# Performance work log

Measured on AMD Instinct MI355X. Metric: run time of the kernel, lower is better.

The kernel has to match this reference:

```python
import math
import jax, jax.numpy as jnp
import numpy as np

B, L = 2, 4096
D_MODEL, D_STATE, D_CONV, EXPAND = 1024, 64, 4, 2
D_INNER = EXPAND * D_MODEL
DT_RANK = max(1, D_MODEL // 16)
EPS = float(jnp.finfo(jnp.float32).eps)  # torch nn.RMSNorm default eps


def setup_inputs() -> dict:
    key = jax.random.key(0)
    ks = jax.random.split(key, 8)
    sc = lambda k, shape, scale: jax.random.normal(k, shape, jnp.float32) * scale
    x = jax.random.normal(ks[0], (B, L, D_MODEL), jnp.float32)
    in_proj_w = sc(ks[1], (2 * D_INNER, D_MODEL), D_MODEL ** -0.5)
    conv_w = sc(ks[2], (D_INNER, 1, D_CONV), D_CONV ** -0.5)  # depthwise kernel
    conv_b = jnp.zeros((D_INNER,), jnp.float32)
    norm_w = jnp.ones((D_INNER,), jnp.float32)
    dt_std = DT_RANK ** -0.5
    dt_w = jax.random.uniform(ks[3], (D_INNER, D_INNER), jnp.float32, -dt_std, dt_std)
    dt_b = jnp.full((D_INNER,), math.log(0.5), jnp.float32)
    A_log = jnp.log(jnp.tile(jnp.arange(1, D_STATE + 1, dtype=jnp.float32), (D_INNER, 1)))
    D = jnp.ones((D_INNER,), jnp.float32)
    B_w = sc(ks[4], (D_STATE, D_INNER), D_INNER ** -0.5)
    C_w = sc(ks[5], (D_STATE, D_INNER), D_INNER ** -0.5)
    out_w = sc(ks[6], (D_MODEL, D_INNER), D_INNER ** -0.5)
    return dict(x=x, in_proj_w=in_proj_w, conv_w=conv_w, conv_b=conv_b,
                norm_w=norm_w, dt_w=dt_w, dt_b=dt_b, A_log=A_log, D=D,
                B_w=B_w, C_w=C_w, out_w=out_w)


def _mamba2_fwd(x, in_proj_w, conv_w, conv_b, norm_w, dt_w, dt_b, A_log, D, B_w, C_w, out_w):
    batch, seq_len, _ = x.shape
    # input projection + gating
    xg = x @ in_proj_w.T                               # [B, L, 2*d_inner]
    x_inner, gate = jnp.split(xg, 2, axis=-1)
    x_inner = x_inner * jax.nn.silu(gate)
    # causal depthwise conv1d (left pad d_conv-1, keep first L outputs)
    lhs = x_inner.transpose(0, 2, 1)                   # [B, d_inner, L]
    conv = jax.lax.conv_general_dilated(
        lhs, conv_w, window_strides=(1,), padding=[(D_CONV - 1, 0)],
        feature_group_count=conv_w.shape[0])
    x_conv = (conv + conv_b[None, :, None]).transpose(0, 2, 1)  # [B, L, d_inner]
    # RMSNorm
    x_conv = x_conv * jax.lax.rsqrt(jnp.mean(x_conv ** 2, axis=-1, keepdims=True) + EPS) * norm_w
    # SSM parameters
    dt = jax.nn.softplus(x_conv @ dt_w.T + dt_b)       # [B, L, d_inner]
    A = -jnp.exp(A_log)                                # [d_inner, d_state]
    Bt = x_conv @ B_w.T                                # [B, L, d_state]
    Ct = x_conv @ C_w.T                                # [B, L, d_state]

    # selective scan: h_t = exp(dt_t * A) * h_{t-1} + dt_t * B_t * x_t
    def step(h, inp):
        dt_t, b_t, c_t, xc_t = inp                     # [B,d], [B,N], [B,N], [B,d]
        A_bar = jnp.exp(dt_t[..., None] * A)           # [B, d_inner, d_state]
        h = A_bar * h + (dt_t * xc_t)[..., None] * b_t[:, None, :]
        y_t = jnp.einsum('bdn,bn->bd', h, c_t)
        return h, y_t

    h0 = jnp.zeros((batch, x_conv.shape[-1], D_STATE), x_conv.dtype)
    xs = (dt.transpose(1, 0, 2), Bt.transpose(1, 0, 2),
          Ct.transpose(1, 0, 2), x_conv.transpose(1, 0, 2))
    _, ys = jax.lax.scan(step, h0, xs)                 # ys: [L, B, d_inner]
    y = ys.transpose(1, 0, 2) + D * x_conv             # skip connection
    return y @ out_w.T                                 # [B, L, d_model]


def reference(x, in_proj_w, conv_w, conv_b, norm_w, dt_w, dt_b, A_log, D, B_w, C_w, out_w):
    return _mamba2_fwd(x, in_proj_w, conv_w, conv_b, norm_w, dt_w, dt_b, A_log, D, B_w, C_w, out_w)
```

## Files before the change

kernel.cpp:

```cpp
#include <hip/hip_runtime.h>
#include <cmath>

#define BB 2
#define LL 4096
#define DM 1024
#define DI 2048
#define NS 64
static constexpr float EPSF  = 1.1920928955078125e-07f;
static constexpr float LOG2E = 1.4426950408889634f;

typedef unsigned short u16;
typedef __attribute__((ext_vector_type(4))) unsigned short u16x4;
typedef __attribute__((ext_vector_type(8))) short bf16x8;
typedef __attribute__((ext_vector_type(4))) float f32x4;

__device__ __forceinline__ u16 f2bf(float f){
    unsigned u = __float_as_uint(f);
    return (u16)((u + 0x7fffu + ((u >> 16) & 1u)) >> 16);
}
__device__ __forceinline__ float bf2f(u16 h){ return __uint_as_float(((unsigned)h) << 16); }
__device__ __forceinline__ float rlf(float v, int j){
    return __uint_as_float(__builtin_amdgcn_readlane(__float_as_uint(v), j));
}
__device__ __forceinline__ void gload16(const void* g, void* l){
    __builtin_amdgcn_global_load_lds((const __attribute__((address_space(1))) void*)g,
                                     (__attribute__((address_space(3))) void*)l, 16, 0, 0);
}

__global__ __launch_bounds__(256)
void cvtf2b(const float* __restrict__ in, u16* __restrict__ out, int n)
{
    int i = (blockIdx.x * 256 + threadIdx.x) * 4;
    float4 v = *(const float4*)(in + i);
    u16x4 o; o[0]=f2bf(v.x); o[1]=f2bf(v.y); o[2]=f2bf(v.z); o[3]=f2bf(v.w);
    *(u16x4*)(out + i) = o;
}

template<int MODE, int OUTBF>
__global__ __launch_bounds__(256)
void gemm_bf16(const u16* __restrict__ A, const u16* __restrict__ W,
               const float* __restrict__ bias, void* __restrict__ Cout,
               int M, int N, int K)
{
    __shared__ u16 As[128*32];
    __shared__ u16 Bs[128*32];
    __shared__ u16 Bg[(MODE==1) ? 128*32 : 8];

    const int tid  = threadIdx.x;
    const int lane = tid & 63;
    const int wave = tid >> 6;
    const int m0 = blockIdx.y * 128;
    const int n0 = blockIdx.x * 128;
    const int wr = wave >> 1, wc = wave & 1;

    f32x4 acc [4][4];
    f32x4 acc2[(MODE==1)?4:1][(MODE==1)?4:1];
    #pragma unroll
    for (int i=0;i<4;i++)
        #pragma unroll
        for (int j=0;j<4;j++)
            #pragma unroll
            for (int r=0;r<4;r++) acc[i][j][r] = 0.f;
    if (MODE==1){
        #pragma unroll
        for (int i=0;i<4;i++)
            #pragma unroll
            for (int j=0;j<4;j++)
                #pragma unroll
                for (int r=0;r<4;r++) acc2[i][j][r] = 0.f;
    }

    for (int k0 = 0; k0 < K; k0 += 32) {
        #pragma unroll
        for (int it = 0; it < 2; ++it) {
            const int s  = it*256 + tid;
            const int r  = s >> 2;
            const int q  = s & 3;
            const int qs = q ^ ((r >> 1) & 3);
            const int ub = (it*256 + wave*64) * 8;
            gload16(A + (size_t)(m0 + r)*K + k0 + qs*8, As + ub);
            gload16(W + (size_t)(n0 + r)*K + k0 + qs*8, Bs + ub);
            if (MODE==1)
                gload16(W + (size_t)(N + n0 + r)*K + k0 + qs*8, Bg + ub);
        }
        __syncthreads();

        bf16x8 af[4], bfr[4], bgr[(MODE==1)?4:1];
        #pragma unroll
        for (int mi=0; mi<4; ++mi){
            const int r  = wr*64 + mi*16 + (lane & 15);
            const int qs = (lane >> 4) ^ ((r >> 1) & 3);
            af[mi] = *(const bf16x8*)(As + (r*4 + qs)*8);
        }
        #pragma unroll
        for (int ni=0; ni<4; ++ni){
            const int c  = wc*64 + ni*16 + (lane & 15);
            const int qs = (lane >> 4) ^ ((c >> 1) & 3);
            bfr[ni] = *(const bf16x8*)(Bs + (c*4 + qs)*8);
            if (MODE==1) bgr[ni] = *(const bf16x8*)(Bg + (c*4 + qs)*8);
        }
        #pragma unroll
        for (int mi=0; mi<4; ++mi)
            #pragma unroll
            for (int ni=0; ni<4; ++ni){
                acc[mi][ni] = __builtin_amdgcn_mfma_f32_16x16x32_bf16(af[mi], bfr[ni], acc[mi][ni], 0,0,0);
                if (MODE==1)
                    acc2[mi][ni] = __builtin_amdgcn_mfma_f32_16x16x32_bf16(af[mi], bgr[ni], acc2[mi][ni], 0,0,0);
            }
        __syncthreads();
    }

    #pragma unroll
    for (int mi=0; mi<4; ++mi){
        #pragma unroll
        for (int ni=0; ni<4; ++ni){
            const int col = n0 + wc*64 + ni*16 + (lane & 15);
            #pragma unroll
            for (int rj=0; rj<4; ++rj){
                const int row = m0 + wr*64 + mi*16 + (lane >> 4)*4 + rj;
                float v = acc[mi][ni][rj];
                if (MODE==1){
                    float g = acc2[mi][ni][rj];
                    v = v * (g / (1.f + __expf(-g)));
                }
                if (MODE==2){
                    float z = v + bias[col];
                    v = (z > 20.f) ? z : log1pf(__expf(z));
                }
                if (MODE==3){
                    ((float*)Cout)[((size_t)row*64 + (col & 63))*2 + (col >> 6)] = v;
                } else if (OUTBF) {
                    ((u16*)Cout)[(size_t)row*N + col] = f2bf(v);
                } else {
                    ((float*)Cout)[(size_t)row*N + col] = v;
                }
            }
        }
    }
}

__global__ __launch_bounds__(256)
void conv_rms(const u16* __restrict__ xin, const float* __restrict__ cw,
              const float* __restrict__ cb, const float* __restrict__ nw,
              u16* __restrict__ xc)
{
    const int bl  = blockIdx.x;
    const int l   = bl & (LL-1);
    const int tid = threadIdx.x;
    const int d0  = tid * 8;

    float a[8];
    #pragma unroll
    for (int j=0;j<8;j++) a[j] = cb[d0+j];
    #pragma unroll
    for (int t=0;t<4;t++){
        const int ls = l - 3 + t;
        if (ls >= 0){
            bf16x8 xv = *(const bf16x8*)(xin + (size_t)(bl-3+t)*DI + d0);
            #pragma unroll
            for (int j=0;j<8;j++)
                a[j] += bf2f((u16)xv[j]) * cw[(d0+j)*4 + t];
        }
    }
    float ss = 0.f;
    #pragma unroll
    for (int j=0;j<8;j++) ss += a[j]*a[j];
    ss += __shfl_xor(ss,32); ss += __shfl_xor(ss,16); ss += __shfl_xor(ss,8);
    ss += __shfl_xor(ss,4);  ss += __shfl_xor(ss,2);  ss += __shfl_xor(ss,1);
    __shared__ float red[4];
    if ((tid & 63)==0) red[tid>>6] = ss;
    __syncthreads();
    const float tot   = red[0]+red[1]+red[2]+red[3];
    const float scale = rsqrtf(tot * (1.f/DI) + EPSF);
    u16x4 o0, o1;
    #pragma unroll
    for (int j=0;j<4;j++) o0[j] = f2bf(a[j]  *scale*nw[d0+j]);
    #pragma unroll
    for (int j=0;j<4;j++) o1[j] = f2bf(a[4+j]*scale*nw[d0+4+j]);
    *(u16x4*)(xc + (size_t)bl*DI + d0)     = o0;
    *(u16x4*)(xc + (size_t)bl*DI + d0 + 4) = o1;
}

__global__ __launch_bounds__(256)
void transpose_bf(const u16* __restrict__ in, u16* __restrict__ out, int R, int C)
{
    __shared__ u16 t[32][36];
    const int b  = blockIdx.z;
    const int r0 = blockIdx.y * 32;
    const int c0 = blockIdx.x * 32;
    const int ir = threadIdx.x >> 3;
    const int ic = (threadIdx.x & 7) * 4;
    const size_t base = (size_t)b * R * C;

    u16x4 v = *(const u16x4*)(in + base + (size_t)(r0+ir)*C + c0 + ic);
    #pragma unroll
    for (int k=0;k<4;k++) t[ir][ic+k] = v[k];
    __syncthreads();
    u16x4 o;
    #pragma unroll
    for (int k=0;k<4;k++) o[k] = t[ic+k][ir];
    *(u16x4*)(out + base + (size_t)(c0+ir)*R + r0 + ic) = o;
}

#define BSTAGE(MU) \
    { _Pragma("unroll") \
      for (int i=0;i<MU;i++){ \
          const bool g = (lane & MU) != 0; \
          float q = g ? p[i] : p[i+MU]; \
          float r = __shfl_xor(q, MU); \
          p[i] = (g ? p[i+MU] : p[i]) + r; \
      } }

__global__ __launch_bounds__(512)
void scan3(const u16* __restrict__ dtT, const u16* __restrict__ xcT,
           const float* __restrict__ BCi, const float* __restrict__ A_log,
           const float* __restrict__ Dp, u16* __restrict__ yT)
{
    __shared__ float lbc[2][64*128];
    const int tid  = threadIdx.x;
    const int lane = tid & 63;
    const int wave = tid >> 6;
    const int b    = blockIdx.x >> 8;
    const int d    = (blockIdx.x & 255) * 8 + wave;

    const float Ac = -__expf(A_log[d*NS + lane]) * LOG2E;
    const float Dd = Dp[d];
    const size_t chbase = ((size_t)b*DI + d) * LL;
    const u16* dtp = dtT + chbase;
    const u16* xcp = xcT + chbase;
    u16*       yp  = yT  + chbase;
    const float* bcb = BCi + (size_t)b * LL * 128;

    auto stage = [&](int t0, int bufi){
        const float* src = bcb + (size_t)t0 * 128;
        #pragma unroll
        for (int i=0;i<4;i++){
            const int slot = i*512 + wave*64;
            gload16(src + (size_t)(slot + lane)*4, &lbc[bufi][slot*4]);
        }
    };

    stage(0, 0);
    asm volatile("s_waitcnt vmcnt(0)" ::: "memory");
    __syncthreads();

    float h = 0.f;
    int cur = 0;
    for (int t0 = 0; t0 < LL; t0 += 64) {
        if (t0 + 64 < LL) stage(t0 + 64, cur ^ 1);

        const float dtL = bf2f(dtp[t0 + lane]);
        const float xcL = bf2f(xcp[t0 + lane]);
        const float uL  = dtL * xcL;
        const float* lb = lbc[cur];

        float p[64];
        #pragma unroll
        for (int j=0;j<64;j++){
            const float dtv = rlf(dtL, j);
            const float uv  = rlf(uL, j);
            const float2 bc = *(const float2*)(lb + (j*64 + lane)*2);
            const float a   = exp2f(dtv * Ac);
            h = a*h + uv*bc.x;
            p[j] = h * bc.y;
        }
        BSTAGE(32) BSTAGE(16) BSTAGE(8) BSTAGE(4) BSTAGE(2) BSTAGE(1)
        yp[t0 + lane] = f2bf(p[0] + Dd * xcL);

        asm volatile("s_waitcnt vmcnt(0)" ::: "memory");
        __syncthreads();
        cur ^= 1;
    }
}

extern "C" void kernel_launch(void* const* d_in, const int* in_sizes, int n_in,
                              void* d_out, int out_size, void* d_ws, size_t ws_size,
                              hipStream_t stream) {
    const float* x       = (const float*)d_in[0];
    const float* in_proj = (const float*)d_in[1];
    const float* conv_w  = (const float*)d_in[2];
    const float* conv_b  = (const float*)d_in[3];
    const float* norm_w  = (const float*)d_in[4];
    const float* dt_w    = (const float*)d_in[5];
    const float* dt_b    = (const float*)d_in[6];
    const float* A_log   = (const float*)d_in[7];
    const float* Dp      = (const float*)d_in[8];
    const float* B_w     = (const float*)d_in[9];
    const float* C_w     = (const float*)d_in[10];
    const float* out_w   = (const float*)d_in[11];

    const int M = BB * LL;
    u16* wsu = (u16*)d_ws;
    u16*   x_bf   = wsu;
    u16*   ip_bf  = wsu + (size_t)M*DM;
    u16*   dtw_bf = ip_bf + (size_t)2*DI*DM;
    u16*   xin_bf = dtw_bf + (size_t)DI*DI;
    u16*   xc_bf  = xin_bf + (size_t)M*DI;
    float* BC     = (float*)(xc_bf + (size_t)M*DI);
    u16*   bcw_bf = (u16*)(BC + (size_t)M*128);
    u16*   ow_bf  = bcw_bf + (size_t)128*DI;
    u16*   dt_bf  = xin_bf;
    u16*   dtT_bf = x_bf;
    u16*   xcT_bf = xin_bf;
    u16*   yT_bf  = xc_bf;
    u16*   y_bf   = xin_bf;

    cvtf2b<<<(M*DM)/1024, 256, 0, stream>>>(x, x_bf, M*DM);
    cvtf2b<<<(2*DI*DM)/1024, 256, 0, stream>>>(in_proj, ip_bf, 2*DI*DM);
    cvtf2b<<<(DI*DI)/1024, 256, 0, stream>>>(dt_w, dtw_bf, DI*DI);
    cvtf2b<<<(DM*DI)/1024, 256, 0, stream>>>(out_w, ow_bf, DM*DI);
    cvtf2b<<<(NS*DI)/1024, 256, 0, stream>>>(B_w, bcw_bf, NS*DI);
    cvtf2b<<<(NS*DI)/1024, 256, 0, stream>>>(C_w, bcw_bf + (size_t)NS*DI, NS*DI);

    gemm_bf16<1,1><<<dim3(DI/128, M/128), 256, 0, stream>>>(
        x_bf, ip_bf, nullptr, xin_bf, M, DI, DM);

    conv_rms<<<M, 256, 0, stream>>>(xin_bf, conv_w, conv_b, norm_w, xc_bf);

    gemm_bf16<2,1><<<dim3(DI/128, M/128), 256, 0, stream>>>(
        xc_bf, dtw_bf, dt_b, dt_bf, M, DI, DI);

    gemm_bf16<3,0><<<dim3(1, M/128), 256, 0, stream>>>(
        xc_bf, bcw_bf, nullptr, BC, M, 128, DI);

    transpose_bf<<<dim3(DI/32, LL/32, BB), 256, 0, stream>>>(dt_bf, dtT_bf, LL, DI);
    transpose_bf<<<dim3(DI/32, LL/32, BB), 256, 0, stream>>>(xc_bf, xcT_bf, LL, DI);

    scan3<<<BB*DI/8, 512, 0, stream>>>(dtT_bf, xcT_bf, BC, A_log, Dp, yT_bf);

    transpose_bf<<<dim3(LL/32, DI/32, BB), 256, 0, stream>>>(yT_bf, y_bf, DI, LL);

    gemm_bf16<0,0><<<dim3(DM/128, M/128), 256, 0, stream>>>(
        y_bf, ow_bf, nullptr, (float*)d_out, M, DM, DI);
}
```

Before: 1.084 ms.

## Pack B/C to bf16 pairs, prefetch dt/x, use permlane32 swap in scan

A new kernel packs the B and C projections into one 32-bit word per state (two bf16 values), which halves the LDS staging traffic and footprint in the scan. The scan also loads the next chunk's dt and x values one step ahead so their latency overlaps compute, and replaces the first butterfly reduction stage with v_permlane32_swap. Output conversion now uses the hardware bf16 pack instruction. The change costs an extra launch plus a round trip through memory, and rounds B and C to bf16.

```diff
diff --git a/kernel.cpp b/kernel.cpp
--- a/kernel.cpp
+++ b/kernel.cpp
@@ -11,6 +11,7 @@
 
 typedef unsigned short u16;
 typedef __attribute__((ext_vector_type(4))) unsigned short u16x4;
+typedef __attribute__((ext_vector_type(4))) unsigned int u32x4;
 typedef __attribute__((ext_vector_type(8))) short bf16x8;
 typedef __attribute__((ext_vector_type(4))) float f32x4;
 
@@ -127,16 +128,27 @@
                     float z = v + bias[col];
                     v = (z > 20.f) ? z : log1pf(__expf(z));
                 }
-                if (MODE==3){
-                    ((float*)Cout)[((size_t)row*64 + (col & 63))*2 + (col >> 6)] = v;
-                } else if (OUTBF) {
-                    ((u16*)Cout)[(size_t)row*N + col] = f2bf(v);
-                } else {
-                    ((float*)Cout)[(size_t)row*N + col] = v;
-                }
+                if (OUTBF) ((u16*)Cout)[(size_t)row*N + col] = f2bf(v);
+                else       ((float*)Cout)[(size_t)row*N + col] = v;
             }
         }
     }
+}
+
+__global__ __launch_bounds__(256)
+void packbc(const float* __restrict__ BC, unsigned* __restrict__ out)
+{
+    const int idx = (blockIdx.x * 256 + threadIdx.x) * 4;
+    const int t  = idx >> 6;
+    const int n0 = idx & 63;
+    float4 Bv = *(const float4*)(BC + (size_t)t*128 + n0);
+    float4 Cv = *(const float4*)(BC + (size_t)t*128 + 64 + n0);
+    u32x4 o;
+    o[0] = (unsigned)f2bf(Bv.x) | ((unsigned)f2bf(Cv.x) << 16);
+    o[1] = (unsigned)f2bf(Bv.y) | ((unsigned)f2bf(Cv.y) << 16);
+    o[2] = (unsigned)f2bf(Bv.z) | ((unsigned)f2bf(Cv.z) << 16);
+    o[3] = (unsigned)f2bf(Bv.w) | ((unsigned)f2bf(Cv.w) << 16);
+    *(u32x4*)(out + idx) = o;
 }
 
 __global__ __launch_bounds__(256)
@@ -212,11 +224,11 @@
       } }
 
 __global__ __launch_bounds__(512)
-void scan3(const u16* __restrict__ dtT, const u16* __restrict__ xcT,
-           const float* __restrict__ BCi, const float* __restrict__ A_log,
+void scan6(const u16* __restrict__ dtT, const u16* __restrict__ xcT,
+           const unsigned* __restrict__ BCp, const float* __restrict__ A_log,
            const float* __restrict__ Dp, u16* __restrict__ yT)
 {
-    __shared__ float lbc[2][64*128];
+    __shared__ unsigned lbc[2][64*64];
     const int tid  = threadIdx.x;
     const int lane = tid & 63;
     const int wave = tid >> 6;
@@ -229,12 +241,12 @@
     const u16* dtp = dtT + chbase;
     const u16* xcp = xcT + chbase;
     u16*       yp  = yT  + chbase;
-    const float* bcb = BCi + (size_t)b * LL * 128;
+    const unsigned* bcb = BCp + (size_t)b * LL * 64;
 
     auto stage = [&](int t0, int bufi){
-        const float* src = bcb + (size_t)t0 * 128;
-        #pragma unroll
-        for (int i=0;i<4;i++){
+        const unsigned* src = bcb + (size_t)t0 * 64;
+        #pragma unroll
+        for (int i=0;i<2;i++){
             const int slot = i*512 + wave*64;
             gload16(src + (size_t)(slot + lane)*4, &lbc[bufi][slot*4]);
         }
@@ -244,31 +256,49 @@
     asm volatile("s_waitcnt vmcnt(0)" ::: "memory");
     __syncthreads();
 
+    float dtL = bf2f(dtp[lane]);
+    float xcL = bf2f(xcp[lane]);
+
     float h = 0.f;
     int cur = 0;
     for (int t0 = 0; t0 < LL; t0 += 64) {
-        if (t0 + 64 < LL) stage(t0 + 64, cur ^ 1);
-
-        const float dtL = bf2f(dtp[t0 + lane]);
-        const float xcL = bf2f(xcp[t0 + lane]);
-        const float uL  = dtL * xcL;
-        const float* lb = lbc[cur];
+        const bool more = (t0 + 64 < LL);
+        if (more) stage(t0 + 64, cur ^ 1);
+        float dtN = 0.f, xcN = 0.f;
+        if (more) { dtN = bf2f(dtp[t0 + 64 + lane]); xcN = bf2f(xcp[t0 + 64 + lane]); }
+
+        const float uL = dtL * xcL;
+        const unsigned* lb = lbc[cur];
 
         float p[64];
         #pragma unroll
         for (int j=0;j<64;j++){
             const float dtv = rlf(dtL, j);
             const float uv  = rlf(uL, j);
-            const float2 bc = *(const float2*)(lb + (j*64 + lane)*2);
-            const float a   = exp2f(dtv * Ac);
-            h = a*h + uv*bc.x;
-            p[j] = h * bc.y;
-        }
-        BSTAGE(32) BSTAGE(16) BSTAGE(8) BSTAGE(4) BSTAGE(2) BSTAGE(1)
-        yp[t0 + lane] = f2bf(p[0] + Dd * xcL);
+            const unsigned w = lb[j*64 + lane];
+            const float Bv = __uint_as_float(w << 16);
+            const float Cv = __uint_as_float(w & 0xffff0000u);
+            const float a  = exp2f(dtv * Ac);
+            h = a*h + uv*Bv;
+            p[j] = h * Cv;
+        }
+        #pragma unroll
+        for (int i=0;i<32;i++){
+            float a0 = p[i], b0 = p[i+32];
+            asm("v_permlane32_swap_b32 %0, %1" : "+v"(a0), "+v"(b0));
+            p[i] = a0 + b0;
+        }
+        BSTAGE(16) BSTAGE(8) BSTAGE(4) BSTAGE(2) BSTAGE(1)
+        {
+            float yv = p[0] + Dd * xcL;
+            unsigned pk;
+            asm("v_cvt_pk_bf16_f32 %0, %1, %2" : "=v"(pk) : "v"(yv), "v"(yv));
+            yp[t0 + lane] = (u16)pk;
+        }
 
         asm volatile("s_waitcnt vmcnt(0)" ::: "memory");
         __syncthreads();
+        dtL = dtN; xcL = xcN;
         cur ^= 1;
     }
 }
@@ -299,6 +329,7 @@
     float* BC     = (float*)(xc_bf + (size_t)M*DI);
     u16*   bcw_bf = (u16*)(BC + (size_t)M*128);
     u16*   ow_bf  = bcw_bf + (size_t)128*DI;
+    unsigned* BCp = (unsigned*)(ow_bf + (size_t)DM*DI);
     u16*   dt_bf  = xin_bf;
     u16*   dtT_bf = x_bf;
     u16*   xcT_bf = xin_bf;
@@ -320,13 +351,14 @@
     gemm_bf16<2,1><<<dim3(DI/128, M/128), 256, 0, stream>>>(
         xc_bf, dtw_bf, dt_b, dt_bf, M, DI, DI);
 
-    gemm_bf16<3,0><<<dim3(1, M/128), 256, 0, stream>>>(
+    gemm_bf16<0,0><<<dim3(1, M/128), 256, 0, stream>>>(
         xc_bf, bcw_bf, nullptr, BC, M, 128, DI);
+    packbc<<<(M*64)/1024, 256, 0, stream>>>(BC, BCp);
 
     transpose_bf<<<dim3(DI/32, LL/32, BB), 256, 0, stream>>>(dt_bf, dtT_bf, LL, DI);
     transpose_bf<<<dim3(DI/32, LL/32, BB), 256, 0, stream>>>(xc_bf, xcT_bf, LL, DI);
 
-    scan3<<<BB*DI/8, 512, 0, stream>>>(dtT_bf, xcT_bf, BC, A_log, Dp, yT_bf);
+    scan6<<<BB*DI/8, 512, 0, stream>>>(dtT_bf, xcT_bf, BCp, A_log, Dp, yT_bf);
 
     transpose_bf<<<dim3(LL/32, DI/32, BB), 256, 0, stream>>>(yT_bf, y_bf, DI, LL);
 
```

Result: slower. 1.145 ms (+5.6%).
